# Kernel tuning notes

Measured on AMD Instinct MI355X. Metric: run time of the kernel, lower is better.

The kernel has to match this reference:

```python
import jax, jax.numpy as jnp
import numpy as np

NUM_GROUPS = 32
EPS = 1e-6


def group_norm(x, gamma, beta):
    # x: [b, c, h, w]
    b, c, h, w = x.shape
    xg = x.reshape(b, NUM_GROUPS, c // NUM_GROUPS, h, w)
    mean = xg.mean(axis=(2, 3, 4), keepdims=True)
    var = xg.var(axis=(2, 3, 4), keepdims=True)
    xn = ((xg - mean) * jax.lax.rsqrt(var + EPS)).reshape(b, c, h, w)
    return xn * gamma[None, :, None, None] + beta[None, :, None, None]


def conv1x1(x, w, bias):
    # 1x1 conv == channel-mixing matmul. x: [b,c,h,w], w: [co,ci]
    y = jnp.einsum('bchw,oc->bohw', x, w)
    return y + bias[None, :, None, None]


def setup_inputs() -> dict:
    key = jax.random.key(0)
    ks = jax.random.split(key, 10)
    B, C, H, W = 4, 512, 64, 64
    s = 1.0 / np.sqrt(C)
    inp = {
        'x': jax.random.normal(ks[0], (B, C, H, W), jnp.float32),
        'gamma': jnp.ones((C,), jnp.float32),
        'beta': jnp.zeros((C,), jnp.float32),
        'wq': jax.random.normal(ks[1], (C, C), jnp.float32) * s,
        'bq': jnp.zeros((C,), jnp.float32),
        'wk': jax.random.normal(ks[2], (C, C), jnp.float32) * s,
        'bk': jnp.zeros((C,), jnp.float32),
        'wv': jax.random.normal(ks[3], (C, C), jnp.float32) * s,
        'bv': jnp.zeros((C,), jnp.float32),
        'wo': jax.random.normal(ks[4], (C, C), jnp.float32) * s,
        'bo': jnp.zeros((C,), jnp.float32),
    }
    return inp


def reference(x, gamma, beta, wq, bq, wk, bk, wv, bv, wo, bo):
    b, c, h, w = x.shape
    h_ = group_norm(x, gamma, beta)
    q = conv1x1(h_, wq, bq).reshape(b, c, h * w)  # [b,c,n]
    k = conv1x1(h_, wk, bk).reshape(b, c, h * w)
    v = conv1x1(h_, wv, bv).reshape(b, c, h * w)
    scale = jnp.asarray(c, x.dtype) ** -0.5
    # scores: [b, n, n] = q^T k
    scores = jnp.einsum('bcn,bcm->bnm', q, k) * scale
    attn = jax.nn.softmax(scores, axis=2)
    # out: [b, c, n] = v @ attn^T  (h_[i] = sum_j attn[i,j] v[j])
    out = jnp.einsum('bnm,bcm->bcn', attn, v).reshape(b, c, h, w)
    out = conv1x1(out, wo, bo)
    return x + out
```

## Files before the change

kernel.cpp:

```cpp
#include <hip/hip_runtime.h>

typedef __bf16 bf16x8 __attribute__((ext_vector_type(8)));
typedef float f32x4 __attribute__((ext_vector_type(4)));
typedef unsigned short u16;

__device__ __forceinline__ u16 f2bf(float f) {
  unsigned int u = __builtin_bit_cast(unsigned int, f);
  u += 0x7fff + ((u >> 16) & 1);
  return (u16)(u >> 16);
}
__device__ __forceinline__ float bf2f(u16 s) {
  unsigned int u = ((unsigned int)s) << 16;
  return __builtin_bit_cast(float, u);
}
__device__ __forceinline__ void unp8(uint4 u, float* f) {
  f[0] = bf2f(u.x & 0xffff); f[1] = bf2f(u.x >> 16);
  f[2] = bf2f(u.y & 0xffff); f[3] = bf2f(u.y >> 16);
  f[4] = bf2f(u.z & 0xffff); f[5] = bf2f(u.z >> 16);
  f[6] = bf2f(u.w & 0xffff); f[7] = bf2f(u.w >> 16);
}
__device__ __forceinline__ uint4 pk8(const float* f) {
  uint4 u;
  u.x = (unsigned)f2bf(f[0]) | ((unsigned)f2bf(f[1]) << 16);
  u.y = (unsigned)f2bf(f[2]) | ((unsigned)f2bf(f[3]) << 16);
  u.z = (unsigned)f2bf(f[4]) | ((unsigned)f2bf(f[5]) << 16);
  u.w = (unsigned)f2bf(f[6]) | ((unsigned)f2bf(f[7]) << 16);
  return u;
}

__device__ __forceinline__ void gl_lds16(const u16* g, u16* l) {
  __builtin_amdgcn_global_load_lds(
      (const __attribute__((address_space(1))) void*)g,
      (__attribute__((address_space(3))) void*)l, 16, 0, 0);
}

__global__ __launch_bounds__(512, 2) void gemm_nt256(
    const u16* __restrict__ A, int lda, unsigned long long sA,
    const u16* __restrict__ Bt, int ldb, unsigned long long sB,
    u16* __restrict__ Cout, int ldc, unsigned long long sC,
    unsigned long long sSplit, int K, float alpha, int tn,
    const float* __restrict__ bias_col) {
  __shared__ u16 lds[2][4][8192];

  const int t = threadIdx.x;
  const int lane = t & 63;
  const int w = t >> 6;
  const int bz = blockIdx.z;
  A  += (size_t)bz * sA + (size_t)blockIdx.y * K;
  Bt += (size_t)bz * sB + (size_t)blockIdx.y * K;
  Cout += (size_t)blockIdx.y * sSplit;

  const int nwg = gridDim.x;
  const int flat = blockIdx.x;
  const int wg = (flat & 7) * (nwg >> 3) + (flat >> 3);
  const int m0 = (wg / tn) * 256;
  const int n0 = (wg % tn) * 256;

  const int NKT = K >> 6;

  const int sr = lane >> 3;
  const int sc = ((lane & 7) ^ sr) * 8;
  const u16* gA = A  + (size_t)(m0 + w * 16 + sr) * lda + sc;
  const u16* gB = Bt + (size_t)(n0 + w * 16 + sr) * ldb + sc;
  const size_t a128 = (size_t)128 * lda, b128 = (size_t)128 * ldb;
  const size_t a8 = (size_t)8 * lda, b8 = (size_t)8 * ldb;
  const int lws = w * 1024;

  auto stage = [&](int slot, int region, int kt) {
    kt = kt < NKT ? kt : NKT - 1;
    u16* l = &lds[slot][region][lws];
    if (region < 2) {
      const u16* g = gA + (region ? a128 : 0) + (size_t)kt * 64;
      gl_lds16(g, l);
      gl_lds16(g + a8, l + 512);
    } else {
      const u16* g = gB + (region == 3 ? b128 : 0) + (size_t)kt * 64;
      gl_lds16(g, l);
      gl_lds16(g + b8, l + 512);
    }
  };

  const int wr = w >> 2, wc = w & 3;
  const int fr = lane & 15, kg = lane >> 4;
  const int frx = (fr & 7) << 4;

  f32x4 acc[8][4] = {};
  bf16x8 af[4][2], bq[2][2];

#define LDA_(s, qm)                                                            \
  {                                                                            \
    const u16* Ab = &lds[s][0][0];                                             \
    _Pragma("unroll") for (int m = 0; m < 4; ++m) {                            \
      const int R = wr * 128 + (qm) * 64 + m * 16 + fr;                        \
      _Pragma("unroll") for (int kk = 0; kk < 2; ++kk)                         \
          af[m][kk] = *reinterpret_cast<const bf16x8*>(                        \
              Ab + R * 64 + (((kk * 64 + kg * 16) ^ frx) >> 1));               \
    }                                                                          \
  }
#define LDB_(s, qn)                                                            \
  {                                                                            \
    const u16* Bb = &lds[s][2][0];                                             \
    _Pragma("unroll") for (int n = 0; n < 2; ++n) {                            \
      const int R = wc * 64 + (qn) * 32 + n * 16 + fr;                         \
      _Pragma("unroll") for (int kk = 0; kk < 2; ++kk)                         \
          bq[n][kk] = *reinterpret_cast<const bf16x8*>(                        \
              Bb + R * 64 + (((kk * 64 + kg * 16) ^ frx) >> 1));               \
    }                                                                          \
  }
#define PH(s, qm, qn, DOA, DOB, ss, rr, kt, VM)                                \
  {                                                                            \
    if (DOA) LDA_(s, qm)                                                       \
    if (DOB) LDB_(s, qn)                                                       \
    stage(ss, rr, kt);                                                         \
    __builtin_amdgcn_s_barrier();                                              \
    asm volatile("s_waitcnt lgkmcnt(0)" ::: "memory");                         \
    __builtin_amdgcn_s_setprio(1);                                             \
    _Pragma("unroll") for (int kk = 0; kk < 2; ++kk)                           \
    _Pragma("unroll") for (int m = 0; m < 4; ++m)                              \
    _Pragma("unroll") for (int n = 0; n < 2; ++n)                              \
        acc[(qm)*4 + m][(qn)*2 + n] = __builtin_amdgcn_mfma_f32_16x16x32_bf16( \
            af[m][kk], bq[n][kk], acc[(qm)*4 + m][(qn)*2 + n], 0, 0, 0);       \
    __builtin_amdgcn_s_setprio(0);                                             \
    if (VM) asm volatile("s_waitcnt vmcnt(2)" ::: "memory");                   \
    __builtin_amdgcn_s_barrier();                                              \
  }

  stage(0, 0, 0); stage(0, 1, 0); stage(0, 2, 0); stage(0, 3, 0);
  stage(1, 0, 1);
  asm volatile("s_waitcnt vmcnt(2)" ::: "memory");
  __builtin_amdgcn_s_barrier();

  for (int j = 0; j < (NKT >> 1); ++j) {
    const int k1 = 2 * j + 1, k2 = 2 * j + 2, k3 = 2 * j + 3;
    PH(0, 0, 0, 1, 1, 1, 1, k1, 0)
    PH(0, 0, 1, 0, 1, 1, 2, k1, 0)
    PH(0, 1, 1, 1, 0, 1, 3, k1, 0)
    PH(0, 1, 0, 0, 1, 0, 0, k2, 1)
    PH(1, 0, 0, 1, 1, 0, 1, k2, 0)
    PH(1, 0, 1, 0, 1, 0, 2, k2, 0)
    PH(1, 1, 1, 1, 0, 0, 3, k2, 0)
    PH(1, 1, 0, 0, 1, 1, 0, k3, 1)
  }
#undef PH
#undef LDB_
#undef LDA_

  __syncthreads();
  u16* cs = &lds[0][0][0];
#pragma unroll
  for (int a = 0; a < 8; ++a)
#pragma unroll
    for (int b = 0; b < 4; ++b) {
      const int col = wc * 64 + b * 16 + fr;
      const float bc = bias_col ? bias_col[n0 + col] : 0.0f;
      const int row = wr * 128 + a * 16 + kg * 4;
#pragma unroll
      for (int r = 0; r < 4; ++r)
        cs[(row + r) * 256 + col] = f2bf(acc[a][b][r] * alpha + bc);
    }
  __syncthreads();
  const size_t cb = (size_t)bz * sC;
#pragma unroll
  for (int it = 0; it < 16; ++it) {
    const int off = (it * 512 + t) * 8;
    const int row = off >> 8, col = off & 255;
    *reinterpret_cast<uint4*>(&Cout[cb + (size_t)(m0 + row) * ldc + (n0 + col)]) =
        *reinterpret_cast<const uint4*>(&cs[off]);
  }
}

template <bool OUT_F32>
__global__ __launch_bounds__(256) void gemm_nt(
    const u16* __restrict__ A, int lda, unsigned long long sA,
    const u16* __restrict__ Bt, int ldb, unsigned long long sB,
    void* __restrict__ Cout, int ldc, unsigned long long sC,
    int K, float alpha,
    const float* __restrict__ bias_row, const float* __restrict__ bias_col,
    const float* __restrict__ residual, unsigned long long sRes) {
  __shared__ u16 lds[128 * 128];
  u16* As = lds;
  u16* Bs = lds + 8192;

  const int t = threadIdx.x;
  const int bz = blockIdx.z;
  A  += (size_t)bz * sA;
  Bt += (size_t)bz * sB;
  const int m0 = blockIdx.x * 128;
  const int n0 = blockIdx.y * 128;

  const int lane = t & 63;
  const int w = t >> 6;

  const int srow = w * 32 + (lane >> 3);
  const int scol = (lane & 7) * 8;
  const u16* gA = A  + (size_t)(m0 + srow) * lda + scol;
  const u16* gB = Bt + (size_t)(n0 + srow) * ldb + scol;
  u16* lA = As + w * 2048;
  u16* lB = Bs + w * 2048;

  f32x4 acc[4][4] = {};
  const int wm = (w >> 1) * 64;
  const int wn = (w & 1) * 64;
  const int fr = lane & 15;
  const int kg = lane >> 4;

  for (int k0 = 0; k0 < K; k0 += 64) {
    __syncthreads();
#pragma unroll
    for (int i = 0; i < 4; ++i) {
      gl_lds16(gA + (size_t)(i * 8) * lda + k0, lA + i * 512);
      gl_lds16(gB + (size_t)(i * 8) * ldb + k0, lB + i * 512);
    }
    __syncthreads();

#pragma unroll
    for (int kk = 0; kk < 2; ++kk) {
      bf16x8 af[4], bfr[4];
#pragma unroll
      for (int m = 0; m < 4; ++m)
        af[m] = *reinterpret_cast<const bf16x8*>(
            &As[(wm + m * 16 + fr) * 64 + kk * 32 + kg * 8]);
#pragma unroll
      for (int n = 0; n < 4; ++n)
        bfr[n] = *reinterpret_cast<const bf16x8*>(
            &Bs[(wn + n * 16 + fr) * 64 + kk * 32 + kg * 8]);
#pragma unroll
      for (int m = 0; m < 4; ++m)
#pragma unroll
        for (int n = 0; n < 4; ++n)
          acc[m][n] = __builtin_amdgcn_mfma_f32_16x16x32_bf16(af[m], bfr[n], acc[m][n], 0, 0, 0);
    }
  }

  const size_t cbase = (size_t)bz * sC;
  const size_t rbase = (size_t)bz * sRes;
  const int rq = kg * 4;

  if (OUT_F32) {
    float* Cf = reinterpret_cast<float*>(Cout);
    float* lf = reinterpret_cast<float*>(lds);
#pragma unroll
    for (int h = 0; h < 2; ++h) {
      __syncthreads();
      if ((wm >> 6) == h) {
#pragma unroll
        for (int m = 0; m < 4; ++m)
#pragma unroll
          for (int n = 0; n < 4; ++n) {
            const float bc = bias_col ? bias_col[n0 + wn + n * 16 + fr] : 0.0f;
#pragma unroll
            for (int r = 0; r < 4; ++r)
              lf[(m * 16 + rq + r) * 128 + (wn + n * 16 + fr)] =
                  acc[m][n][r] * alpha + bc;
          }
      }
      __syncthreads();
#pragma unroll
      for (int it = 0; it < 8; ++it) {
        const int off = (it * 256 + t) * 4;
        const int row = off >> 7, col = off & 127;
        const int grow = m0 + h * 64 + row, gcol = n0 + col;
        float4 v = *reinterpret_cast<const float4*>(&lf[off]);
        if (bias_row) {
          const float br = bias_row[grow];
          v.x += br; v.y += br; v.z += br; v.w += br;
        }
        if (residual) {
          const float4 rx = *reinterpret_cast<const float4*>(
              &residual[rbase + (size_t)grow * ldc + gcol]);
          v.x += rx.x; v.y += rx.y; v.z += rx.z; v.w += rx.w;
        }
        *reinterpret_cast<float4*>(&Cf[cbase + (size_t)grow * ldc + gcol]) = v;
      }
    }
  } else {
    __syncthreads();
#pragma unroll
    for (int m = 0; m < 4; ++m) {
#pragma unroll
      for (int n = 0; n < 4; ++n) {
        const int gcol = n0 + wn + n * 16 + fr;
        const float bc = bias_col ? bias_col[gcol] : 0.0f;
#pragma unroll
        for (int r = 0; r < 4; ++r) {
          const int grow = m0 + wm + m * 16 + rq + r;
          float v = acc[m][n][r] * alpha + bc;
          if (bias_row) v += bias_row[grow];
          lds[(wm + m * 16 + rq + r) * 128 + (wn + n * 16 + fr)] = f2bf(v);
        }
      }
    }
    __syncthreads();
    u16* Cb = reinterpret_cast<u16*>(Cout);
#pragma unroll
    for (int j = 0; j < 8; ++j) {
      const int off = (j * 256 + t) * 8;
      const int row = off >> 7, col = off & 127;
      *reinterpret_cast<uint4*>(&Cb[cbase + (size_t)(m0 + row) * ldc + (n0 + col)]) =
          *reinterpret_cast<const uint4*>(&lds[off]);
    }
  }
}

__global__ __launch_bounds__(256) void groupnorm_k(
    const float* __restrict__ x, const float* __restrict__ gamma,
    const float* __restrict__ beta, u16* __restrict__ h_t, int C, int N) {
  const int g = blockIdx.x;
  const int b = blockIdx.y;
  const int t = threadIdx.x;
  const float* xb = x + ((size_t)b * C + g * 16) * N;

  float s = 0.f, q = 0.f;
  for (int c = 0; c < 16; ++c) {
    const float4* xr = reinterpret_cast<const float4*>(xb + (size_t)c * N);
    for (int j = t; j < N / 4; j += 256) {
      float4 v = xr[j];
      s += v.x + v.y + v.z + v.w;
      q += v.x * v.x + v.y * v.y + v.z * v.z + v.w * v.w;
    }
  }
#pragma unroll
  for (int o = 32; o > 0; o >>= 1) { s += __shfl_down(s, o); q += __shfl_down(q, o); }
  __shared__ float rs[4], rqs[4], stats[2];
  const int lane = t & 63, wid = t >> 6;
  if (lane == 0) { rs[wid] = s; rqs[wid] = q; }
  __syncthreads();
  if (t == 0) {
    float S = rs[0] + rs[1] + rs[2] + rs[3];
    float Q = rqs[0] + rqs[1] + rqs[2] + rqs[3];
    const float inv = 1.0f / (16.0f * (float)N);
    float mean = S * inv;
    float var = Q * inv - mean * mean;
    stats[0] = mean;
    stats[1] = rsqrtf(var + 1e-6f);
  }
  __syncthreads();
  const float mean = stats[0], rstd = stats[1];

  float gm[16], bt[16];
#pragma unroll
  for (int c = 0; c < 16; ++c) {
    gm[c] = gamma[g * 16 + c] * rstd;
    bt[c] = beta[g * 16 + c] - mean * gm[c];
  }
  u16* ho = h_t + (size_t)b * N * C + g * 16;
  for (int n = t; n < N; n += 256) {
    union { u16 us[16]; uint4 v4[2]; } pk;
#pragma unroll
    for (int c = 0; c < 16; ++c) {
      float v = xb[(size_t)c * N + n];
      pk.us[c] = f2bf(v * gm[c] + bt[c]);
    }
    uint4* dst = reinterpret_cast<uint4*>(ho + (size_t)n * C);
    dst[0] = pk.v4[0];
    dst[1] = pk.v4[1];
  }
}

__global__ __launch_bounds__(256) void softmax_rows(u16* __restrict__ S) {
  const size_t row = (size_t)blockIdx.y * gridDim.x + blockIdx.x;
  uint4* rp4 = reinterpret_cast<uint4*>(S + row * 4096);
  const int t = threadIdx.x;
  uint4 u0 = rp4[t], u1 = rp4[t + 256];
  float f[16];
  unp8(u0, f); unp8(u1, f + 8);

  float mx = f[0];
#pragma unroll
  for (int i = 1; i < 16; ++i) mx = fmaxf(mx, f[i]);
#pragma unroll
  for (int o = 32; o > 0; o >>= 1) mx = fmaxf(mx, __shfl_down(mx, o));
  __shared__ float red[4], bc[2];
  const int lane = t & 63, wid = t >> 6;
  if (lane == 0) red[wid] = mx;
  __syncthreads();
  if (t == 0) bc[0] = fmaxf(fmaxf(red[0], red[1]), fmaxf(red[2], red[3]));
  __syncthreads();
  mx = bc[0];

  float sum = 0.f;
#pragma unroll
  for (int i = 0; i < 16; ++i) { f[i] = __expf(f[i] - mx); sum += f[i]; }
#pragma unroll
  for (int o = 32; o > 0; o >>= 1) sum += __shfl_down(sum, o);
  if (lane == 0) red[wid] = sum;
  __syncthreads();
  if (t == 0) bc[1] = 1.0f / (red[0] + red[1] + red[2] + red[3]);
  __syncthreads();
  const float inv = bc[1];
#pragma unroll
  for (int i = 0; i < 16; ++i) f[i] *= inv;
  rp4[t] = pk8(f);
  rp4[t + 256] = pk8(f + 8);
}

__global__ __launch_bounds__(256) void wcvt(const float* __restrict__ src,
                                            u16* __restrict__ dst, int n) {
  const int i = (blockIdx.x * 256 + threadIdx.x) * 8;
  if (i >= n) return;
  const float4* s4 = reinterpret_cast<const float4*>(src + i);
  float4 a = s4[0], b = s4[1];
  float f[8] = {a.x, a.y, a.z, a.w, b.x, b.y, b.z, b.w};
  *reinterpret_cast<uint4*>(dst + i) = pk8(f);
}

__global__ __launch_bounds__(256) void reduce_pv(const u16* __restrict__ p,
                                                 u16* __restrict__ o, int n) {
  const int i = (blockIdx.x * 256 + threadIdx.x) * 8;
  if (i >= n) return;
  uint4 a = *reinterpret_cast<const uint4*>(p + i);
  uint4 b = *reinterpret_cast<const uint4*>(p + n + i);
  float fa[8], fb[8];
  unp8(a, fa); unp8(b, fb);
#pragma unroll
  for (int j = 0; j < 8; ++j) fa[j] += fb[j];
  *reinterpret_cast<uint4*>(o + i) = pk8(fa);
}

__global__ __launch_bounds__(256) void bcat2(const float* __restrict__ a,
                                             const float* __restrict__ b,
                                             float* __restrict__ o, int n) {
  const int i = blockIdx.x * 256 + threadIdx.x;
  if (i < n) o[i] = a[i];
  else if (i < 2 * n) o[i] = b[i - n];
}

extern "C" void kernel_launch(void* const* d_in, const int* in_sizes, int n_in,
                              void* d_out, int out_size, void* d_ws, size_t ws_size,
                              hipStream_t stream) {
  const float* x     = (const float*)d_in[0];
  const float* gamma = (const float*)d_in[1];
  const float* beta  = (const float*)d_in[2];
  const float* wq    = (const float*)d_in[3];
  const float* bq    = (const float*)d_in[4];
  const float* wk    = (const float*)d_in[5];
  const float* bk    = (const float*)d_in[6];
  const float* wv    = (const float*)d_in[7];
  const float* bv    = (const float*)d_in[8];
  const float* wo    = (const float*)d_in[9];
  const float* bo    = (const float*)d_in[10];

  const int B = 4, C = 512, N = 4096;
  const size_t NC = (size_t)N * C;
  const size_t NN = (size_t)N * N;
  const size_t CC = (size_t)C * C;

  char* ws = (char*)d_ws;
  size_t off = 0;
  auto alloc = [&](size_t bytes) {
    size_t r = off;
    off = (off + bytes + 255) & ~(size_t)255;
    return r;
  };
  u16* wq_b = (u16*)(ws + alloc(CC * 2));
  u16* wk_b = (u16*)(ws + alloc(CC * 2));
  u16* wv_b = (u16*)(ws + alloc(CC * 2));
  u16* wo_b = (u16*)(ws + alloc(CC * 2));
  float* bqk = (float*)(ws + alloc(1024 * 4));
  u16* h_t  = (u16*)(ws + alloc(B * NC * 2));
  u16* qk_t = (u16*)(ws + alloc(B * N * 1024 * 2));
  u16* v_cn = (u16*)(ws + alloc(B * NC * 2));
  u16* o_t  = (u16*)(ws + alloc(B * NC * 2));
  const size_t base_need = off;

  int s_batched = 0;
  u16* S;
  if (ws_size >= base_need + B * NN * 2) {
    S = (u16*)(ws + alloc(B * NN * 2));
    s_batched = 1;
  } else if (ws_size >= base_need + NN * 2) {
    S = (u16*)(ws + alloc(NN * 2));
  } else {
    S = (u16*)d_out;
  }
  u16* o_part = qk_t;

  wcvt<<<dim3(CC / 2048), 256, 0, stream>>>(wq, wq_b, (int)CC);
  wcvt<<<dim3(CC / 2048), 256, 0, stream>>>(wk, wk_b, (int)CC);
  wcvt<<<dim3(CC / 2048), 256, 0, stream>>>(wv, wv_b, (int)CC);
  wcvt<<<dim3(CC / 2048), 256, 0, stream>>>(wo, wo_b, (int)CC);
  bcat2<<<dim3(4), 256, 0, stream>>>(bq, bk, bqk, C);

  groupnorm_k<<<dim3(32, B), 256, 0, stream>>>(x, gamma, beta, h_t, C, N);

  gemm_nt256<<<dim3((N / 256) * (1024 / 256), 1, B), 512, 0, stream>>>(
      h_t, C, NC, wq_b, C, 0, qk_t, 1024, (unsigned long long)N * 1024, 0,
      C, 1.0f, 1024 / 256, bqk);
  dim3 gv(C / 128, N / 128, B);
  gemm_nt<false><<<gv, 256, 0, stream>>>(wv_b, C, 0, h_t, C, NC, v_cn, N, NC,
                                         C, 1.0f, bv, nullptr, nullptr, 0);

  const float scale = 0.044194173824159216f;
  if (s_batched) {
    gemm_nt256<<<dim3((N / 256) * (N / 256), 1, B), 512, 0, stream>>>(
        qk_t, 1024, (unsigned long long)N * 1024, qk_t + 512, 1024,
        (unsigned long long)N * 1024, S, N, NN, 0, C, scale, N / 256, nullptr);
    softmax_rows<<<dim3(N, B), 256, 0, stream>>>(S);
    gemm_nt256<<<dim3((N / 256) * (C / 256), 2, B), 512, 0, stream>>>(
        S, N, NN, v_cn, N, NC, o_part, C, NC, (unsigned long long)B * NC,
        N / 2, 1.0f, C / 256, nullptr);
    reduce_pv<<<dim3((int)(B * NC / 2048)), 256, 0, stream>>>(o_part, o_t, (int)(B * NC));
  } else {
    for (int b = 0; b < B; ++b) {
      gemm_nt256<<<dim3((N / 256) * (N / 256), 1, 1), 512, 0, stream>>>(
          qk_t + (size_t)b * N * 1024, 1024, 0, qk_t + (size_t)b * N * 1024 + 512,
          1024, 0, S, N, 0, 0, C, scale, N / 256, nullptr);
      softmax_rows<<<dim3(N, 1), 256, 0, stream>>>(S);
      gemm_nt256<<<dim3((N / 256) * (C / 256), 1, 1), 512, 0, stream>>>(
          S, N, 0, v_cn + (size_t)b * NC, N, 0, o_t + (size_t)b * NC, C, 0, 0,
          N, 1.0f, C / 256, nullptr);
    }
  }

  dim3 gf(C / 128, N / 128, B);
  gemm_nt<true><<<gf, 256, 0, stream>>>(wo_b, C, 0, o_t, C, NC, d_out, N, NC,
                                        C, 1.0f, bo, nullptr, x, NC);
}
```

Baseline: 329.8 us.

## Replace materialized attention with split-KV flash attention and combine kernel

Replaces the QK^T GEMM, row softmax, split PV GEMM and reduction with a fused flash-attention kernel that streams K and V tiles through double-buffered LDS with online softmax, and splits the KV range in two across blocks mapped by XCD. A combine kernel merges the two partial outputs using saved max and sum values. This removes writing and reading the full N×N score matrix and several launches. In exchange it adds conditional rescaling (skipped when the max grows by at most 8), float partial outputs, and a grid of only 256 blocks, which could limit occupancy.

Result: slower. 469.3 us (+42.3%).

```diff
diff --git a/kernel.cpp b/kernel.cpp
--- a/kernel.cpp
+++ b/kernel.cpp
@@ -12,12 +12,6 @@
 __device__ __forceinline__ float bf2f(u16 s) {
   unsigned int u = ((unsigned int)s) << 16;
   return __builtin_bit_cast(float, u);
-}
-__device__ __forceinline__ void unp8(uint4 u, float* f) {
-  f[0] = bf2f(u.x & 0xffff); f[1] = bf2f(u.x >> 16);
-  f[2] = bf2f(u.y & 0xffff); f[3] = bf2f(u.y >> 16);
-  f[4] = bf2f(u.z & 0xffff); f[5] = bf2f(u.z >> 16);
-  f[6] = bf2f(u.w & 0xffff); f[7] = bf2f(u.w >> 16);
 }
 __device__ __forceinline__ uint4 pk8(const float* f) {
   uint4 u;
@@ -32,6 +26,205 @@
   __builtin_amdgcn_global_load_lds(
       (const __attribute__((address_space(1))) void*)g,
       (__attribute__((address_space(3))) void*)l, 16, 0, 0);
+}
+
+#define FA_KV 32
+
+__global__ __launch_bounds__(512, 2) void flash_attn(
+    const u16* __restrict__ qk, const u16* __restrict__ vcn,
+    float* __restrict__ Opart, float2* __restrict__ mlout, int N) {
+  __shared__ u16 Kb[2][FA_KV][512];
+  __shared__ u16 Vb[2][512][FA_KV];
+  __shared__ u16 Pb[128][FA_KV];
+  __shared__ float Fac[128];
+  __shared__ int Flag[128];
+
+  const int t = threadIdx.x, lane = t & 63, w = t >> 6;
+  const int fr = lane & 15, kg = lane >> 4;
+
+  const int fl = blockIdx.x + (blockIdx.y << 5) + (blockIdx.z << 6);
+  const int xcd = fl & 7, qb = fl >> 3;
+  const int split = xcd >> 2, bz = xcd & 3;
+  const int kv0 = split * (N >> 1);
+  const int nsteps = (N >> 1) / FA_KV;
+
+  const u16* qkb = qk + (size_t)bz * N * 1024;
+  const u16* vb  = vcn + (size_t)bz * 512 * N;
+
+  bf16x8 qf[16];
+  {
+    const u16* qp = qkb + (size_t)(qb * 128 + w * 16 + fr) * 1024 + kg * 8;
+#pragma unroll
+    for (int kk = 0; kk < 16; ++kk)
+      qf[kk] = *reinterpret_cast<const bf16x8*>(qp + kk * 32);
+  }
+
+  f32x4 o[8][4] = {};
+  float m_[4], l_[4];
+#pragma unroll
+  for (int r = 0; r < 4; ++r) { m_[r] = -1e30f; l_[r] = 0.f; }
+
+  const float c1 = 0.06376694396f;
+
+  auto stageK = [&](int buf, int s) {
+#pragma unroll
+    for (int j = 0; j < 4; ++j) {
+      const int row = w * 4 + j;
+      const u16* g = qkb + (size_t)(kv0 + s * FA_KV + row) * 1024 + 512 +
+                     ((lane ^ (row & 7)) << 3);
+      gl_lds16(g, &Kb[buf][row][0]);
+    }
+  };
+  auto stageV = [&](int buf, int s) {
+#pragma unroll
+    for (int j = 0; j < 4; ++j) {
+      const int r0 = w * 64 + j * 16;
+      const int row = r0 + (lane >> 2);
+      const u16* g = vb + (size_t)row * N + kv0 + s * FA_KV +
+                     (((lane & 3) ^ (row & 3)) << 3);
+      gl_lds16(g, &Vb[buf][r0][0]);
+    }
+  };
+
+  if (t < 128) Flag[t] = 0;
+  stageK(0, 0); stageV(0, 0);
+  asm volatile("s_waitcnt vmcnt(0) lgkmcnt(0)" ::: "memory");
+  __builtin_amdgcn_sched_barrier(0);
+  __builtin_amdgcn_s_barrier();
+
+  for (int s = 0; s < nsteps; ++s) {
+    const int cb = s & 1;
+    if (s + 1 < nsteps) { stageK(cb ^ 1, s + 1); stageV(cb ^ 1, s + 1); }
+
+    f32x4 sv0 = {}, sv1 = {};
+#pragma unroll
+    for (int kk = 0; kk < 16; ++kk) {
+      bf16x8 k0 = *reinterpret_cast<const bf16x8*>(
+          &Kb[cb][fr][0] + ((((kk << 2) | kg) ^ (fr & 7)) << 3));
+      bf16x8 k1 = *reinterpret_cast<const bf16x8*>(
+          &Kb[cb][16 + fr][0] + ((((kk << 2) | kg) ^ (fr & 7)) << 3));
+      sv0 = __builtin_amdgcn_mfma_f32_16x16x32_bf16(qf[kk], k0, sv0, 0, 0, 0);
+      sv1 = __builtin_amdgcn_mfma_f32_16x16x32_bf16(qf[kk], k1, sv1, 0, 0, 0);
+    }
+
+    float u0[4], u1[4], pmax[4];
+#pragma unroll
+    for (int r = 0; r < 4; ++r) {
+      u0[r] = sv0[r] * c1; u1[r] = sv1[r] * c1;
+      pmax[r] = fmaxf(u0[r], u1[r]);
+#pragma unroll
+      for (int msk = 1; msk < 16; msk <<= 1)
+        pmax[r] = fmaxf(pmax[r], __shfl_xor(pmax[r], msk));
+    }
+    const bool okl = (pmax[0] - m_[0] <= 8.f) & (pmax[1] - m_[1] <= 8.f) &
+                     (pmax[2] - m_[2] <= 8.f) & (pmax[3] - m_[3] <= 8.f);
+    const bool allok = __all(okl);
+    float fac[4];
+    if (allok) {
+      fac[0] = fac[1] = fac[2] = fac[3] = 1.f;
+    } else {
+#pragma unroll
+      for (int r = 0; r < 4; ++r) {
+        const float nm = fmaxf(m_[r], pmax[r]);
+        fac[r] = exp2f(m_[r] - nm);
+        m_[r] = nm;
+      }
+      if (lane == 0) Flag[s] = 1;
+    }
+    u16* pbase = &Pb[0][0];
+    float rs[4];
+#pragma unroll
+    for (int r = 0; r < 4; ++r) {
+      const float p0 = exp2f(u0[r] - m_[r]);
+      const float p1 = exp2f(u1[r] - m_[r]);
+      rs[r] = p0 + p1;
+      const int row = w * 16 + (kg << 2) + r;
+      const int rx = row & 3;
+      pbase[row * 32 + (((fr >> 3) ^ rx) << 3) + (fr & 7)] = f2bf(p0);
+      pbase[row * 32 + (((2 | (fr >> 3)) ^ rx) << 3) + (fr & 7)] = f2bf(p1);
+#pragma unroll
+      for (int msk = 1; msk < 16; msk <<= 1) rs[r] += __shfl_xor(rs[r], msk);
+      l_[r] = l_[r] * fac[r] + rs[r];
+    }
+    if (fr == 0) {
+#pragma unroll
+      for (int r = 0; r < 4; ++r) Fac[w * 16 + (kg << 2) + r] = fac[r];
+    }
+
+    asm volatile("s_waitcnt lgkmcnt(0)" ::: "memory");
+    __builtin_amdgcn_sched_barrier(0);
+    __builtin_amdgcn_s_barrier();
+
+    if (Flag[s] != 0) {
+#pragma unroll
+      for (int ms = 0; ms < 8; ++ms) {
+        const float4 fv = *reinterpret_cast<const float4*>(&Fac[ms * 16 + (kg << 2)]);
+#pragma unroll
+        for (int ns = 0; ns < 4; ++ns) {
+          o[ms][ns][0] *= fv.x; o[ms][ns][1] *= fv.y;
+          o[ms][ns][2] *= fv.z; o[ms][ns][3] *= fv.w;
+        }
+      }
+    }
+    bf16x8 vf[4];
+#pragma unroll
+    for (int ns = 0; ns < 4; ++ns) {
+      const int row = w * 64 + ns * 16 + fr;
+      vf[ns] = *reinterpret_cast<const bf16x8*>(
+          &Vb[cb][row][0] + ((kg ^ (row & 3)) << 3));
+    }
+#pragma unroll
+    for (int ms = 0; ms < 8; ++ms) {
+      const int row = ms * 16 + fr;
+      const bf16x8 pa = *reinterpret_cast<const bf16x8*>(
+          &Pb[row][0] + ((kg ^ (row & 3)) << 3));
+#pragma unroll
+      for (int ns = 0; ns < 4; ++ns)
+        o[ms][ns] = __builtin_amdgcn_mfma_f32_16x16x32_bf16(pa, vf[ns], o[ms][ns], 0, 0, 0);
+    }
+
+    asm volatile("s_waitcnt vmcnt(0)" ::: "memory");
+    __builtin_amdgcn_sched_barrier(0);
+    __builtin_amdgcn_s_barrier();
+  }
+
+  float* op = Opart + (((size_t)split * 4 + bz) * N + qb * 128) * 512 + w * 64;
+#pragma unroll
+  for (int ms = 0; ms < 8; ++ms)
+#pragma unroll
+    for (int ns = 0; ns < 4; ++ns) {
+      const int col = ns * 16 + fr;
+#pragma unroll
+      for (int r = 0; r < 4; ++r)
+        op[(size_t)(ms * 16 + (kg << 2) + r) * 512 + col] = o[ms][ns][r];
+    }
+  if (fr == 0) {
+    float2* mlp = mlout + ((size_t)split * 4 + bz) * N + qb * 128 + w * 16 + (kg << 2);
+#pragma unroll
+    for (int r = 0; r < 4; ++r) mlp[r] = make_float2(m_[r], l_[r]);
+  }
+}
+
+__global__ __launch_bounds__(256) void flash_combine(
+    const float* __restrict__ Opart, const float2* __restrict__ ml,
+    u16* __restrict__ o_t, int total) {
+  const int row = blockIdx.x * 4 + (threadIdx.x >> 6);
+  const int lane = threadIdx.x & 63;
+  const size_t half = (size_t)total * 512;
+  const float2 a = ml[row], b = ml[total + row];
+  const float m = fmaxf(a.x, b.x);
+  float e1 = exp2f(a.x - m), e2 = exp2f(b.x - m);
+  const float inv = 1.f / (a.y * e1 + b.y * e2);
+  e1 *= inv; e2 *= inv;
+  const float* p1 = Opart + (size_t)row * 512 + lane * 8;
+  const float* p2 = p1 + half;
+  const float4 x0 = *(const float4*)p1, x1 = *(const float4*)(p1 + 4);
+  const float4 y0 = *(const float4*)p2, y1 = *(const float4*)(p2 + 4);
+  float f[8] = {x0.x * e1 + y0.x * e2, x0.y * e1 + y0.y * e2,
+                x0.z * e1 + y0.z * e2, x0.w * e1 + y0.w * e2,
+                x1.x * e1 + y1.x * e2, x1.y * e1 + y1.y * e2,
+                x1.z * e1 + y1.z * e2, x1.w * e1 + y1.w * e2};
+  *reinterpret_cast<uint4*>(o_t + (size_t)row * 512 + lane * 8) = pk8(f);
 }
 
 __global__ __launch_bounds__(512, 2) void gemm_nt256(
@@ -159,12 +352,12 @@
         cs[(row + r) * 256 + col] = f2bf(acc[a][b][r] * alpha + bc);
     }
   __syncthreads();
-  const size_t cb = (size_t)bz * sC;
+  const size_t cbs = (size_t)bz * sC;
 #pragma unroll
   for (int it = 0; it < 16; ++it) {
     const int off = (it * 512 + t) * 8;
     const int row = off >> 8, col = off & 255;
-    *reinterpret_cast<uint4*>(&Cout[cb + (size_t)(m0 + row) * ldc + (n0 + col)]) =
+    *reinterpret_cast<uint4*>(&Cout[cbs + (size_t)(m0 + row) * ldc + (n0 + col)]) =
         *reinterpret_cast<const uint4*>(&cs[off]);
   }
 }
@@ -357,43 +550,6 @@
   }
 }
 
-__global__ __launch_bounds__(256) void softmax_rows(u16* __restrict__ S) {
-  const size_t row = (size_t)blockIdx.y * gridDim.x + blockIdx.x;
-  uint4* rp4 = reinterpret_cast<uint4*>(S + row * 4096);
-  const int t = threadIdx.x;
-  uint4 u0 = rp4[t], u1 = rp4[t + 256];
-  float f[16];
-  unp8(u0, f); unp8(u1, f + 8);
-
-  float mx = f[0];
-#pragma unroll
-  for (int i = 1; i < 16; ++i) mx = fmaxf(mx, f[i]);
-#pragma unroll
-  for (int o = 32; o > 0; o >>= 1) mx = fmaxf(mx, __shfl_down(mx, o));
-  __shared__ float red[4], bc[2];
-  const int lane = t & 63, wid = t >> 6;
-  if (lane == 0) red[wid] = mx;
-  __syncthreads();
-  if (t == 0) bc[0] = fmaxf(fmaxf(red[0], red[1]), fmaxf(red[2], red[3]));
-  __syncthreads();
-  mx = bc[0];
-
-  float sum = 0.f;
-#pragma unroll
-  for (int i = 0; i < 16; ++i) { f[i] = __expf(f[i] - mx); sum += f[i]; }
-#pragma unroll
-  for (int o = 32; o > 0; o >>= 1) sum += __shfl_down(sum, o);
-  if (lane == 0) red[wid] = sum;
-  __syncthreads();
-  if (t == 0) bc[1] = 1.0f / (red[0] + red[1] + red[2] + red[3]);
-  __syncthreads();
-  const float inv = bc[1];
-#pragma unroll
-  for (int i = 0; i < 16; ++i) f[i] *= inv;
-  rp4[t] = pk8(f);
-  rp4[t + 256] = pk8(f + 8);
-}
-
 __global__ __launch_bounds__(256) void wcvt(const float* __restrict__ src,
                                             u16* __restrict__ dst, int n) {
   const int i = (blockIdx.x * 256 + threadIdx.x) * 8;
@@ -402,19 +558,6 @@
   float4 a = s4[0], b = s4[1];
   float f[8] = {a.x, a.y, a.z, a.w, b.x, b.y, b.z, b.w};
   *reinterpret_cast<uint4*>(dst + i) = pk8(f);
-}
-
-__global__ __launch_bounds__(256) void reduce_pv(const u16* __restrict__ p,
-                                                 u16* __restrict__ o, int n) {
-  const int i = (blockIdx.x * 256 + threadIdx.x) * 8;
-  if (i >= n) return;
-  uint4 a = *reinterpret_cast<const uint4*>(p + i);
-  uint4 b = *reinterpret_cast<const uint4*>(p + n + i);
-  float fa[8], fb[8];
-  unp8(a, fa); unp8(b, fb);
-#pragma unroll
-  for (int j = 0; j < 8; ++j) fa[j] += fb[j];
-  *reinterpret_cast<uint4*>(o + i) = pk8(fa);
 }
 
 __global__ __launch_bounds__(256) void bcat2(const float* __restrict__ a,
@@ -442,7 +585,6 @@
 
   const int B = 4, C = 512, N = 4096;
   const size_t NC = (size_t)N * C;
-  const size_t NN = (size_t)N * N;
   const size_t CC = (size_t)C * C;
 
   char* ws = (char*)d_ws;
@@ -461,19 +603,8 @@
   u16* qk_t = (u16*)(ws + alloc(B * N * 1024 * 2));
   u16* v_cn = (u16*)(ws + alloc(B * NC * 2));
   u16* o_t  = (u16*)(ws + alloc(B * NC * 2));
-  const size_t base_need = off;
-
-  int s_batched = 0;
-  u16* S;
-  if (ws_size >= base_need + B * NN * 2) {
-    S = (u16*)(ws + alloc(B * NN * 2));
-    s_batched = 1;
-  } else if (ws_size >= base_need + NN * 2) {
-    S = (u16*)(ws + alloc(NN * 2));
-  } else {
-    S = (u16*)d_out;
-  }
-  u16* o_part = qk_t;
+  float*  Opart = (float*)(ws + alloc(2 * B * NC * 4));
+  float2* mlb   = (float2*)(ws + alloc(2 * (size_t)B * N * 8));
 
   wcvt<<<dim3(CC / 2048), 256, 0, stream>>>(wq, wq_b, (int)CC);
   wcvt<<<dim3(CC / 2048), 256, 0, stream>>>(wk, wk_b, (int)CC);
@@ -490,27 +621,8 @@
   gemm_nt<false><<<gv, 256, 0, stream>>>(wv_b, C, 0, h_t, C, NC, v_cn, N, NC,
                                          C, 1.0f, bv, nullptr, nullptr, 0);
 
-  const float scale = 0.044194173824159216f;
-  if (s_batched) {
-    gemm_nt256<<<dim3((N / 256) * (N / 256), 1, B), 512, 0, stream>>>(
-        qk_t, 1024, (unsigned long long)N * 1024, qk_t + 512, 1024,
-        (unsigned long long)N * 1024, S, N, NN, 0, C, scale, N / 256, nullptr);
-    softmax_rows<<<dim3(N, B), 256, 0, stream>>>(S);
-    gemm_nt256<<<dim3((N / 256) * (C / 256), 2, B), 512, 0, stream>>>(
-        S, N, NN, v_cn, N, NC, o_part, C, NC, (unsigned long long)B * NC,
-        N / 2, 1.0f, C / 256, nullptr);
-    reduce_pv<<<dim3((int)(B * NC / 2048)), 256, 0, stream>>>(o_part, o_t, (int)(B * NC));
-  } else {
-    for (int b = 0; b < B; ++b) {
-      gemm_nt256<<<dim3((N / 256) * (N / 256), 1, 1), 512, 0, stream>>>(
-          qk_t + (size_t)b * N * 1024, 1024, 0, qk_t + (size_t)b * N * 1024 + 512,
-          1024, 0, S, N, 0, 0, C, scale, N / 256, nullptr);
-      softmax_rows<<<dim3(N, 1), 256, 0, stream>>>(S);
-      gemm_nt256<<<dim3((N / 256) * (C / 256), 1, 1), 512, 0, stream>>>(
-          S, N, 0, v_cn + (size_t)b * NC, N, 0, o_t + (size_t)b * NC, C, 0, 0,
-          N, 1.0f, C / 256, nullptr);
-    }
-  }
+  flash_attn<<<dim3(32, 2, B), 512, 0, stream>>>(qk_t, v_cn, Opart, mlb, N);
+  flash_combine<<<dim3(B * N / 4), 256, 0, stream>>>(Opart, mlb, o_t, B * N);
 
   dim3 gf(C / 128, N / 128, B);
   gemm_nt<true><<<gf, 256, 0, stream>>>(wo_b, C, 0, o_t, C, NC, d_out, N, NC,
```

## Fuse unnormalized exp into QK^T epilogue and defer softmax normalization

Applied to the files above, without the earlier changes.

The QK^T GEMM epilogue now writes exp2(score*scale*log2e) directly as bf16 and stores per-tile row partial sums. A small kernel reduces these into inverse row sums, and the inverse is applied after the PV GEMM inside the split-K reduce or a new scale kernel. This drops the separate softmax pass, which read and wrote the full B*N*N score matrix. It skips max subtraction, so it relies on scores staying small enough that exp neither overflows nor loses bf16 precision.

Result: no change. 334.4 us (+1.4%).

```diff
diff --git a/kernel.cpp b/kernel.cpp
--- a/kernel.cpp
+++ b/kernel.cpp
@@ -39,8 +39,9 @@
     const u16* __restrict__ Bt, int ldb, unsigned long long sB,
     u16* __restrict__ Cout, int ldc, unsigned long long sC,
     unsigned long long sSplit, int K, float alpha, int tn,
-    const float* __restrict__ bias_col) {
+    const float* __restrict__ bias_col, float* __restrict__ psum) {
   __shared__ u16 lds[2][4][8192];
+  __shared__ float part[4][256];
 
   const int t = threadIdx.x;
   const int lane = t & 63;
@@ -147,25 +148,55 @@
 
   __syncthreads();
   u16* cs = &lds[0][0][0];
-#pragma unroll
-  for (int a = 0; a < 8; ++a)
-#pragma unroll
-    for (int b = 0; b < 4; ++b) {
-      const int col = wc * 64 + b * 16 + fr;
-      const float bc = bias_col ? bias_col[n0 + col] : 0.0f;
-      const int row = wr * 128 + a * 16 + kg * 4;
-#pragma unroll
-      for (int r = 0; r < 4; ++r)
-        cs[(row + r) * 256 + col] = f2bf(acc[a][b][r] * alpha + bc);
-    }
+  if (psum) {
+#pragma unroll
+    for (int a = 0; a < 8; ++a) {
+      const int row = wr * 128 + a * 16 + (kg << 2);
+      float sr_[4] = {0.f, 0.f, 0.f, 0.f};
+#pragma unroll
+      for (int b = 0; b < 4; ++b) {
+        const int col = wc * 64 + b * 16 + fr;
+#pragma unroll
+        for (int r = 0; r < 4; ++r) {
+          const float p = exp2f(acc[a][b][r] * alpha);
+          sr_[r] += p;
+          cs[(row + r) * 256 + col] = f2bf(p);
+        }
+      }
+#pragma unroll
+      for (int r = 0; r < 4; ++r) {
+#pragma unroll
+        for (int msk = 1; msk < 16; msk <<= 1)
+          sr_[r] += __shfl_xor(sr_[r], msk);
+        if (fr == 0) part[wc][row + r] = sr_[r];
+      }
+    }
+  } else {
+#pragma unroll
+    for (int a = 0; a < 8; ++a)
+#pragma unroll
+      for (int b = 0; b < 4; ++b) {
+        const int col = wc * 64 + b * 16 + fr;
+        const float bc = bias_col ? bias_col[n0 + col] : 0.0f;
+        const int row = wr * 128 + a * 16 + (kg << 2);
+#pragma unroll
+        for (int r = 0; r < 4; ++r)
+          cs[(row + r) * 256 + col] = f2bf(acc[a][b][r] * alpha + bc);
+      }
+  }
   __syncthreads();
-  const size_t cb = (size_t)bz * sC;
+  const size_t cbs = (size_t)bz * sC;
 #pragma unroll
   for (int it = 0; it < 16; ++it) {
     const int off = (it * 512 + t) * 8;
     const int row = off >> 8, col = off & 255;
-    *reinterpret_cast<uint4*>(&Cout[cb + (size_t)(m0 + row) * ldc + (n0 + col)]) =
+    *reinterpret_cast<uint4*>(&Cout[cbs + (size_t)(m0 + row) * ldc + (n0 + col)]) =
         *reinterpret_cast<const uint4*>(&cs[off]);
+  }
+  if (psum && t < 256) {
+    const int Mrows = (nwg / tn) << 8;
+    psum[((size_t)bz * tn + (n0 >> 8)) * Mrows + m0 + t] =
+        part[0][t] + part[1][t] + part[2][t] + part[3][t];
   }
 }
 
@@ -357,43 +388,6 @@
   }
 }
 
-__global__ __launch_bounds__(256) void softmax_rows(u16* __restrict__ S) {
-  const size_t row = (size_t)blockIdx.y * gridDim.x + blockIdx.x;
-  uint4* rp4 = reinterpret_cast<uint4*>(S + row * 4096);
-  const int t = threadIdx.x;
-  uint4 u0 = rp4[t], u1 = rp4[t + 256];
-  float f[16];
-  unp8(u0, f); unp8(u1, f + 8);
-
-  float mx = f[0];
-#pragma unroll
-  for (int i = 1; i < 16; ++i) mx = fmaxf(mx, f[i]);
-#pragma unroll
-  for (int o = 32; o > 0; o >>= 1) mx = fmaxf(mx, __shfl_down(mx, o));
-  __shared__ float red[4], bc[2];
-  const int lane = t & 63, wid = t >> 6;
-  if (lane == 0) red[wid] = mx;
-  __syncthreads();
-  if (t == 0) bc[0] = fmaxf(fmaxf(red[0], red[1]), fmaxf(red[2], red[3]));
-  __syncthreads();
-  mx = bc[0];
-
-  float sum = 0.f;
-#pragma unroll
-  for (int i = 0; i < 16; ++i) { f[i] = __expf(f[i] - mx); sum += f[i]; }
-#pragma unroll
-  for (int o = 32; o > 0; o >>= 1) sum += __shfl_down(sum, o);
-  if (lane == 0) red[wid] = sum;
-  __syncthreads();
-  if (t == 0) bc[1] = 1.0f / (red[0] + red[1] + red[2] + red[3]);
-  __syncthreads();
-  const float inv = bc[1];
-#pragma unroll
-  for (int i = 0; i < 16; ++i) f[i] *= inv;
-  rp4[t] = pk8(f);
-  rp4[t + 256] = pk8(f + 8);
-}
-
 __global__ __launch_bounds__(256) void wcvt(const float* __restrict__ src,
                                             u16* __restrict__ dst, int n) {
   const int i = (blockIdx.x * 256 + threadIdx.x) * 8;
@@ -404,25 +398,53 @@
   *reinterpret_cast<uint4*>(dst + i) = pk8(f);
 }
 
-__global__ __launch_bounds__(256) void reduce_pv(const u16* __restrict__ p,
-                                                 u16* __restrict__ o, int n) {
-  const int i = (blockIdx.x * 256 + threadIdx.x) * 8;
-  if (i >= n) return;
-  uint4 a = *reinterpret_cast<const uint4*>(p + i);
-  uint4 b = *reinterpret_cast<const uint4*>(p + n + i);
-  float fa[8], fb[8];
-  unp8(a, fa); unp8(b, fb);
-#pragma unroll
-  for (int j = 0; j < 8; ++j) fa[j] += fb[j];
-  *reinterpret_cast<uint4*>(o + i) = pk8(fa);
-}
-
 __global__ __launch_bounds__(256) void bcat2(const float* __restrict__ a,
                                              const float* __restrict__ b,
                                              float* __restrict__ o, int n) {
   const int i = blockIdx.x * 256 + threadIdx.x;
   if (i < n) o[i] = a[i];
   else if (i < 2 * n) o[i] = b[i - n];
+}
+
+__global__ __launch_bounds__(256) void sumred(const float* __restrict__ psum,
+                                              float* __restrict__ invl,
+                                              int nt, int rows, int total) {
+  const int i = blockIdx.x * 256 + threadIdx.x;
+  if (i >= total) return;
+  const int b = i / rows, n = i - b * rows;
+  const float* p = psum + (size_t)b * nt * rows + n;
+  float s = 0.f;
+  for (int c = 0; c < nt; ++c) s += p[(size_t)c * rows];
+  invl[i] = 1.0f / s;
+}
+
+__global__ __launch_bounds__(256) void reduce_pv(const u16* __restrict__ p,
+                                                 const float* __restrict__ invl,
+                                                 u16* __restrict__ o, int n) {
+  const int i = (blockIdx.x * 256 + threadIdx.x) * 8;
+  if (i >= n) return;
+  const float il = invl[i >> 9];
+  uint4 a = *reinterpret_cast<const uint4*>(p + i);
+  uint4 b = *reinterpret_cast<const uint4*>(p + n + i);
+  float fa[8], fb[8];
+  unp8(a, fa); unp8(b, fb);
+#pragma unroll
+  for (int j = 0; j < 8; ++j) fa[j] = (fa[j] + fb[j]) * il;
+  *reinterpret_cast<uint4*>(o + i) = pk8(fa);
+}
+
+__global__ __launch_bounds__(256) void scale_o(u16* __restrict__ o,
+                                               const float* __restrict__ invl,
+                                               int n) {
+  const int i = (blockIdx.x * 256 + threadIdx.x) * 8;
+  if (i >= n) return;
+  const float il = invl[i >> 9];
+  uint4 a = *reinterpret_cast<const uint4*>(o + i);
+  float fa[8];
+  unp8(a, fa);
+#pragma unroll
+  for (int j = 0; j < 8; ++j) fa[j] *= il;
+  *reinterpret_cast<uint4*>(o + i) = pk8(fa);
 }
 
 extern "C" void kernel_launch(void* const* d_in, const int* in_sizes, int n_in,
@@ -461,6 +483,8 @@
   u16* qk_t = (u16*)(ws + alloc(B * N * 1024 * 2));
   u16* v_cn = (u16*)(ws + alloc(B * NC * 2));
   u16* o_t  = (u16*)(ws + alloc(B * NC * 2));
+  float* psum = (float*)(ws + alloc((size_t)B * 16 * N * 4));
+  float* invl = (float*)(ws + alloc((size_t)B * N * 4));
   const size_t base_need = off;
 
   int s_batched = 0;
@@ -468,10 +492,8 @@
   if (ws_size >= base_need + B * NN * 2) {
     S = (u16*)(ws + alloc(B * NN * 2));
     s_batched = 1;
-  } else if (ws_size >= base_need + NN * 2) {
+  } else {
     S = (u16*)(ws + alloc(NN * 2));
-  } else {
-    S = (u16*)d_out;
   }
   u16* o_part = qk_t;
 
@@ -485,31 +507,33 @@
 
   gemm_nt256<<<dim3((N / 256) * (1024 / 256), 1, B), 512, 0, stream>>>(
       h_t, C, NC, wq_b, C, 0, qk_t, 1024, (unsigned long long)N * 1024, 0,
-      C, 1.0f, 1024 / 256, bqk);
+      C, 1.0f, 1024 / 256, bqk, nullptr);
   dim3 gv(C / 128, N / 128, B);
   gemm_nt<false><<<gv, 256, 0, stream>>>(wv_b, C, 0, h_t, C, NC, v_cn, N, NC,
                                          C, 1.0f, bv, nullptr, nullptr, 0);
 
-  const float scale = 0.044194173824159216f;
+  const float c1 = 0.06376694387439652f;
   if (s_batched) {
     gemm_nt256<<<dim3((N / 256) * (N / 256), 1, B), 512, 0, stream>>>(
         qk_t, 1024, (unsigned long long)N * 1024, qk_t + 512, 1024,
-        (unsigned long long)N * 1024, S, N, NN, 0, C, scale, N / 256, nullptr);
-    softmax_rows<<<dim3(N, B), 256, 0, stream>>>(S);
+        (unsigned long long)N * 1024, S, N, NN, 0, C, c1, N / 256, nullptr, psum);
+    sumred<<<dim3(B * N / 256), 256, 0, stream>>>(psum, invl, 16, N, B * N);
     gemm_nt256<<<dim3((N / 256) * (C / 256), 2, B), 512, 0, stream>>>(
         S, N, NN, v_cn, N, NC, o_part, C, NC, (unsigned long long)B * NC,
-        N / 2, 1.0f, C / 256, nullptr);
-    reduce_pv<<<dim3((int)(B * NC / 2048)), 256, 0, stream>>>(o_part, o_t, (int)(B * NC));
+        N / 2, 1.0f, C / 256, nullptr, nullptr);
+    reduce_pv<<<dim3((int)(B * NC / 2048)), 256, 0, stream>>>(
+        o_part, invl, o_t, (int)(B * NC));
   } else {
     for (int b = 0; b < B; ++b) {
       gemm_nt256<<<dim3((N / 256) * (N / 256), 1, 1), 512, 0, stream>>>(
           qk_t + (size_t)b * N * 1024, 1024, 0, qk_t + (size_t)b * N * 1024 + 512,
-          1024, 0, S, N, 0, 0, C, scale, N / 256, nullptr);
-      softmax_rows<<<dim3(N, 1), 256, 0, stream>>>(S);
+          1024, 0, S, N, 0, 0, C, c1, N / 256, nullptr, psum + (size_t)b * 16 * N);
       gemm_nt256<<<dim3((N / 256) * (C / 256), 1, 1), 512, 0, stream>>>(
           S, N, 0, v_cn + (size_t)b * NC, N, 0, o_t + (size_t)b * NC, C, 0, 0,
-          N, 1.0f, C / 256, nullptr);
-    }
+          N, 1.0f, C / 256, nullptr, nullptr);
+    }
+    sumred<<<dim3(B * N / 256), 256, 0, stream>>>(psum, invl, 16, N, B * N);
+    scale_o<<<dim3((int)(B * NC / 2048)), 256, 0, stream>>>(o_t, invl, (int)(B * NC));
   }
 
   dim3 gf(C / 128, N / 128, B);
```
